# Kernel tuning notes

Hardware: AMD Instinct MI355X
Metric: run time of the kernel (lower is better)

Reference implementation:

```python
import jax, jax.numpy as jnp
import numpy as np

B, T, D, H = 4, 2048, 2048, 16
HD = D // H  # 128
EPS = 1e-5


def setup_inputs() -> dict:
    key = jax.random.key(0)
    ks = jax.random.split(key, 16)
    s_in = 1.0 / np.sqrt(D)
    s_ff = 1.0 / np.sqrt(4 * D)
    return {
        "x": jax.random.normal(ks[0], (B, T, D), jnp.float32),
        # per-head q/k/v projections stacked over heads: [H, D, HD]
        "Wq": jax.random.normal(ks[1], (H, D, HD), jnp.float32) * s_in,
        "bq": jnp.zeros((H, HD), jnp.float32),
        "Wk": jax.random.normal(ks[2], (H, D, HD), jnp.float32) * s_in,
        "bk": jnp.zeros((H, HD), jnp.float32),
        "Wv": jax.random.normal(ks[3], (H, D, HD), jnp.float32) * s_in,
        "bv": jnp.zeros((H, HD), jnp.float32),
        # feed-forward
        "W1": jax.random.normal(ks[4], (D, 4 * D), jnp.float32) * s_in,
        "b1": jnp.zeros((4 * D,), jnp.float32),
        "W2": jax.random.normal(ks[5], (4 * D, D), jnp.float32) * s_ff,
        "b2": jnp.zeros((D,), jnp.float32),
        # layer norms
        "g1": jnp.ones((D,), jnp.float32),
        "be1": jnp.zeros((D,), jnp.float32),
        "g2": jnp.ones((D,), jnp.float32),
        "be2": jnp.zeros((D,), jnp.float32),
    }


def _layernorm(x, g, b):
    mu = jnp.mean(x, axis=-1, keepdims=True)
    var = jnp.mean(jnp.square(x - mu), axis=-1, keepdims=True)
    return (x - mu) * jax.lax.rsqrt(var + EPS) * g + b


def reference(x, Wq, bq, Wk, bk, Wv, bv, W1, b1, W2, b2, g1, be1, g2, be2):
    h = _layernorm(x, g1, be1)
    # per-head projections: [B, H, T, HD]
    q = jnp.einsum("btd,hde->bhte", h, Wq) + bq[None, :, None, :]
    k = jnp.einsum("btd,hde->bhte", h, Wk) + bk[None, :, None, :]
    v = jnp.einsum("btd,hde->bhte", h, Wv) + bv[None, :, None, :]
    scale = 1.0 / jnp.sqrt(jnp.asarray(HD, q.dtype))
    logits = jnp.einsum("bhte,bhse->bhts", q, k) * scale  # [B,H,T,T]
    causal = jnp.tril(jnp.ones((T, T), bool))
    logits = jnp.where(causal[None, None], logits, -jnp.inf)
    attn = jax.nn.softmax(logits, axis=-1)
    out = jnp.einsum("bhts,bhse->bhte", attn, v)  # [B,H,T,HD]
    # concat heads in head order -> [B,T,D]
    out = out.transpose(0, 2, 1, 3).reshape(B, T, D)
    x = x + out
    h2 = _layernorm(x, g2, be2)
    ff = jax.nn.relu(h2 @ W1 + b1) @ W2 + b2
    return x + ff
```

## Files before the change

### kernel.cpp

```cpp
#include <hip/hip_runtime.h>
#include <stdint.h>

#define TLEN 2048
#define DDIM 2048
#define NHEAD 16
#define HDIM 128
#define BSZ 4

typedef short bf16x8 __attribute__((ext_vector_type(8)));
typedef float f32x4 __attribute__((ext_vector_type(4)));

__device__ __forceinline__ unsigned short f32_bf16(float f) {
  union { float f; unsigned int u; } v; v.f = f;
  unsigned int u = v.u;
  unsigned int r = (u + 0x7fffu + ((u >> 16) & 1u)) >> 16;
  return (unsigned short)r;
}

__device__ __forceinline__ void async_cp16(const void* g, void* l) {
  __builtin_amdgcn_global_load_lds(
      (const __attribute__((address_space(1))) unsigned int*)g,
      (__attribute__((address_space(3))) unsigned int*)l, 16, 0, 0);
}

__global__ __launch_bounds__(256) void transpose_bf16_kernel(
    const float* __restrict__ in, unsigned short* __restrict__ out,
    int R, int C, long in_z, long out_z) {
  __shared__ float tile[32][33];
  in += (long)blockIdx.z * in_z;
  out += (long)blockIdx.z * out_z;
  int c0 = blockIdx.x * 32, r0 = blockIdx.y * 32;
  int cr = threadIdx.x & 31, rr = threadIdx.x >> 5;
#pragma unroll
  for (int i = 0; i < 4; ++i)
    tile[rr + i * 8][cr] = in[(long)(r0 + rr + i * 8) * C + c0 + cr];
  __syncthreads();
#pragma unroll
  for (int i = 0; i < 4; ++i)
    out[(long)(c0 + rr + i * 8) * R + r0 + cr] = f32_bf16(tile[cr][rr + i * 8]);
}

__device__ __forceinline__ void block_reduce2(float& s, float& q) {
#pragma unroll
  for (int off = 32; off >= 1; off >>= 1) {
    s += __shfl_xor(s, off);
    q += __shfl_xor(q, off);
  }
  __shared__ float rs[4], rq[4];
  int lane = threadIdx.x & 63, wid = threadIdx.x >> 6;
  if (lane == 0) { rs[wid] = s; rq[wid] = q; }
  __syncthreads();
  s = rs[0] + rs[1] + rs[2] + rs[3];
  q = rq[0] + rq[1] + rq[2] + rq[3];
}

__global__ __launch_bounds__(256) void ln_kernel(
    const float* __restrict__ x, const float* __restrict__ g,
    const float* __restrict__ be, unsigned short* __restrict__ hb) {
  int row = blockIdx.x, tid = threadIdx.x;
  const float* xr = x + (long)row * DDIM;
  float4 v0 = *(const float4*)(xr + tid * 4);
  float4 v1 = *(const float4*)(xr + 1024 + tid * 4);
  float s = v0.x + v0.y + v0.z + v0.w + v1.x + v1.y + v1.z + v1.w;
  float q = v0.x * v0.x + v0.y * v0.y + v0.z * v0.z + v0.w * v0.w +
            v1.x * v1.x + v1.y * v1.y + v1.z * v1.z + v1.w * v1.w;
  block_reduce2(s, q);
  float mu = s * (1.0f / DDIM);
  float var = q * (1.0f / DDIM) - mu * mu;
  float rstd = rsqrtf(var + 1e-5f);
  float4 g0 = *(const float4*)(g + tid * 4);
  float4 g1v = *(const float4*)(g + 1024 + tid * 4);
  float4 b0 = *(const float4*)(be + tid * 4);
  float4 b1v = *(const float4*)(be + 1024 + tid * 4);
  ushort4 o0, o1;
  o0.x = f32_bf16((v0.x - mu) * rstd * g0.x + b0.x);
  o0.y = f32_bf16((v0.y - mu) * rstd * g0.y + b0.y);
  o0.z = f32_bf16((v0.z - mu) * rstd * g0.z + b0.z);
  o0.w = f32_bf16((v0.w - mu) * rstd * g0.w + b0.w);
  o1.x = f32_bf16((v1.x - mu) * rstd * g1v.x + b1v.x);
  o1.y = f32_bf16((v1.y - mu) * rstd * g1v.y + b1v.y);
  o1.z = f32_bf16((v1.z - mu) * rstd * g1v.z + b1v.z);
  o1.w = f32_bf16((v1.w - mu) * rstd * g1v.w + b1v.w);
  *(ushort4*)(hb + (long)row * DDIM + tid * 4) = o0;
  *(ushort4*)(hb + (long)row * DDIM + 1024 + tid * 4) = o1;
}

__global__ __launch_bounds__(256) void resid_ln_kernel(
    const float* __restrict__ x, float* xa,
    const float* __restrict__ g, const float* __restrict__ be,
    unsigned short* __restrict__ hb) {
  int row = blockIdx.x, tid = threadIdx.x;
  const float* xr = x + (long)row * DDIM;
  float* ar = xa + (long)row * DDIM;
  float4 v0 = *(const float4*)(xr + tid * 4);
  float4 a0 = *(const float4*)(ar + tid * 4);
  float4 v1 = *(const float4*)(xr + 1024 + tid * 4);
  float4 a1 = *(const float4*)(ar + 1024 + tid * 4);
  v0.x += a0.x; v0.y += a0.y; v0.z += a0.z; v0.w += a0.w;
  v1.x += a1.x; v1.y += a1.y; v1.z += a1.z; v1.w += a1.w;
  *(float4*)(ar + tid * 4) = v0;
  *(float4*)(ar + 1024 + tid * 4) = v1;
  float s = v0.x + v0.y + v0.z + v0.w + v1.x + v1.y + v1.z + v1.w;
  float q = v0.x * v0.x + v0.y * v0.y + v0.z * v0.z + v0.w * v0.w +
            v1.x * v1.x + v1.y * v1.y + v1.z * v1.z + v1.w * v1.w;
  block_reduce2(s, q);
  float mu = s * (1.0f / DDIM);
  float var = q * (1.0f / DDIM) - mu * mu;
  float rstd = rsqrtf(var + 1e-5f);
  float4 g0 = *(const float4*)(g + tid * 4);
  float4 g1v = *(const float4*)(g + 1024 + tid * 4);
  float4 b0 = *(const float4*)(be + tid * 4);
  float4 b1v = *(const float4*)(be + 1024 + tid * 4);
  ushort4 o0, o1;
  o0.x = f32_bf16((v0.x - mu) * rstd * g0.x + b0.x);
  o0.y = f32_bf16((v0.y - mu) * rstd * g0.y + b0.y);
  o0.z = f32_bf16((v0.z - mu) * rstd * g0.z + b0.z);
  o0.w = f32_bf16((v0.w - mu) * rstd * g0.w + b0.w);
  o1.x = f32_bf16((v1.x - mu) * rstd * g1v.x + b1v.x);
  o1.y = f32_bf16((v1.y - mu) * rstd * g1v.y + b1v.y);
  o1.z = f32_bf16((v1.z - mu) * rstd * g1v.z + b1v.z);
  o1.w = f32_bf16((v1.w - mu) * rstd * g1v.w + b1v.w);
  *(ushort4*)(hb + (long)row * DDIM + tid * 4) = o0;
  *(ushort4*)(hb + (long)row * DDIM + 1024 + tid * 4) = o1;
}

__device__ __forceinline__ void gemm_core(const unsigned short* __restrict__ A,
                                          const unsigned short* __restrict__ Bt,
                                          int K, int lda, int ldb, int m0, int n0,
                                          f32x4 acc[4][4]) {
  __shared__ unsigned short sA[128 * 64];
  __shared__ unsigned short sB[128 * 64];
  const int tid = threadIdx.x;
  const int lane = tid & 63, wid = tid >> 6;
  const int wm = (wid & 1) * 64, wn = (wid >> 1) * 64;
  const int lm = lane & 15, lq = lane >> 4;
#pragma unroll
  for (int mi = 0; mi < 4; ++mi)
#pragma unroll
    for (int ni = 0; ni < 4; ++ni)
      acc[mi][ni] = (f32x4){0.f, 0.f, 0.f, 0.f};
  const int rbase = wid * 32;
  const int ri = lane >> 3;
  const int kgl = lane & 7;
  const int nk = K >> 6;
  for (int kt = 0; kt < nk; ++kt) {
    const unsigned short* Ak = A + (long)m0 * lda + (long)kt * 64;
    const unsigned short* Bk = Bt + (long)n0 * ldb + (long)kt * 64;
#pragma unroll
    for (int ins = 0; ins < 4; ++ins) {
      int row = rbase + ins * 8 + ri;
      int kg = kgl ^ (row & 7);
      async_cp16(Ak + (long)row * lda + kg * 8, &sA[(rbase + ins * 8) * 64]);
      async_cp16(Bk + (long)row * ldb + kg * 8, &sB[(rbase + ins * 8) * 64]);
    }
    __syncthreads();
#pragma unroll
    for (int kc = 0; kc < 2; ++kc) {
      bf16x8 af[4], bfr[4];
#pragma unroll
      for (int mi = 0; mi < 4; ++mi) {
        int row = wm + mi * 16 + lm;
        int kg = (kc * 4 + lq) ^ (row & 7);
        af[mi] = *(const bf16x8*)(&sA[row * 64 + kg * 8]);
      }
#pragma unroll
      for (int ni = 0; ni < 4; ++ni) {
        int row = wn + ni * 16 + lm;
        int kg = (kc * 4 + lq) ^ (row & 7);
        bfr[ni] = *(const bf16x8*)(&sB[row * 64 + kg * 8]);
      }
#pragma unroll
      for (int mi = 0; mi < 4; ++mi)
#pragma unroll
        for (int ni = 0; ni < 4; ++ni)
          acc[mi][ni] = __builtin_amdgcn_mfma_f32_16x16x32_bf16(af[mi], bfr[ni], acc[mi][ni], 0, 0, 0);
    }
    __syncthreads();
  }
}

__global__ __launch_bounds__(256) void gemm_qkv_kernel(
    const unsigned short* __restrict__ A, const unsigned short* __restrict__ WT,
    unsigned short* __restrict__ Qb, unsigned short* __restrict__ Kb,
    unsigned short* __restrict__ VTb,
    const float* __restrict__ bq, const float* __restrict__ bk,
    const float* __restrict__ bv) {
  int m0 = blockIdx.x * 128, n0 = blockIdx.y * 128;
  int z = blockIdx.z;
  const unsigned short* Bt = WT + (long)z * DDIM * DDIM;
  f32x4 acc[4][4];
  gemm_core(A, Bt, DDIM, DDIM, DDIM, m0, n0, acc);
  const float* bias = (z == 0) ? bq : (z == 1) ? bk : bv;
  int lane = threadIdx.x & 63, wid = threadIdx.x >> 6;
  int wm = (wid & 1) * 64, wn = (wid >> 1) * 64, lm = lane & 15, lq = lane >> 4;
  int h = n0 >> 7;
#pragma unroll
  for (int mi = 0; mi < 4; ++mi) {
    int rowb = m0 + wm + mi * 16 + lq * 4;
    int b = rowb >> 11, t0 = rowb & (TLEN - 1);
#pragma unroll
    for (int ni = 0; ni < 4; ++ni) {
      int col = n0 + wn + ni * 16 + lm;
      int e = col & (HDIM - 1);
      float bsv = bias[col];
      if (z < 2) {
        unsigned short* o = (z == 0) ? Qb : Kb;
        long base = ((long)(b * NHEAD + h) * TLEN + t0) * HDIM + e;
#pragma unroll
        for (int r = 0; r < 4; ++r)
          o[base + (long)r * HDIM] = f32_bf16(acc[mi][ni][r] + bsv);
      } else {
        long base = ((long)(b * NHEAD + h) * HDIM + e) * TLEN + t0;
        ushort4 pk;
        pk.x = f32_bf16(acc[mi][ni][0] + bsv);
        pk.y = f32_bf16(acc[mi][ni][1] + bsv);
        pk.z = f32_bf16(acc[mi][ni][2] + bsv);
        pk.w = f32_bf16(acc[mi][ni][3] + bsv);
        *(ushort4*)(VTb + base) = pk;
      }
    }
  }
}

template <int MODE>
__global__ __launch_bounds__(256) void gemm_ffn_kernel(
    const unsigned short* __restrict__ A, const unsigned short* __restrict__ Bt,
    void* __restrict__ outv, const float* __restrict__ bias,
    int K, int lda, int ldb, int N) {
  int m0 = blockIdx.x * 128, n0 = blockIdx.y * 128;
  f32x4 acc[4][4];
  gemm_core(A, Bt, K, lda, ldb, m0, n0, acc);
  int lane = threadIdx.x & 63, wid = threadIdx.x >> 6;
  int wm = (wid & 1) * 64, wn = (wid >> 1) * 64, lm = lane & 15, lq = lane >> 4;
#pragma unroll
  for (int mi = 0; mi < 4; ++mi) {
    int rowb = m0 + wm + mi * 16 + lq * 4;
#pragma unroll
    for (int ni = 0; ni < 4; ++ni) {
      int col = n0 + wn + ni * 16 + lm;
      float bsv = (MODE == 2) ? 0.f : bias[col];
#pragma unroll
      for (int r = 0; r < 4; ++r) {
        long idx = (long)(rowb + r) * N + col;
        float v = acc[mi][ni][r] + bsv;
        if (MODE == 0) {
          ((unsigned short*)outv)[idx] = f32_bf16(v > 0.f ? v : 0.f);
        } else {
          float* o = (float*)outv;
          o[idx] = o[idx] + v;
        }
      }
    }
  }
}

__global__ __launch_bounds__(256, 3) void attn_kernel(
    const unsigned short* __restrict__ Qb, const unsigned short* __restrict__ Kb,
    const unsigned short* __restrict__ VTb, float* __restrict__ Ob) {
  __shared__ __align__(16) char smem[49152];
  unsigned short* kbuf0 = (unsigned short*)smem;
  unsigned short* kbuf1 = (unsigned short*)(smem + 16384);
  unsigned short* sV = (unsigned short*)(smem + 32768);
  const int tid = threadIdx.x, lane = tid & 63, wid = tid >> 6;
  const int lm = lane & 15, lq = lane >> 4;
  int flat = blockIdx.x;
  int swz = (flat & 7) * 256 + (flat >> 3);
  int m5 = swz & 31;
  int bxx = (m5 & 1) ? (m5 >> 1) : (31 - (m5 >> 1));
  int h = (swz >> 5) & 15;
  int b = swz >> 9;
  const int q0 = bxx * 64;
  const long bh = (long)(b * NHEAD + h);
  const unsigned short* qp = Qb + (bh * TLEN + q0 + wid * 16) * HDIM;
  const unsigned short* kp = Kb + bh * TLEN * HDIM;
  const unsigned short* vp = VTb + bh * HDIM * TLEN;
  bf16x8 qf[4];
#pragma unroll
  for (int c = 0; c < 4; ++c)
    qf[c] = *(const bf16x8*)(qp + (long)lm * HDIM + c * 32 + lq * 8);
  f32x4 oacc[8];
#pragma unroll
  for (int c = 0; c < 8; ++c) oacc[c] = (f32x4){0.f, 0.f, 0.f, 0.f};
  float mr[4], lr[4];
#pragma unroll
  for (int r = 0; r < 4; ++r) { mr[r] = -3.0e38f; lr[r] = 0.f; }
  const float sl = 0.08838834764831845f * 1.4426950408889634f;
  const int nk = bxx + 1;
  const int kri = lane >> 4, krg = lane & 15;
  const int vri = lane >> 3, vrg = lane & 7;
#pragma unroll
  for (int i = 0; i < 4; ++i) {
    int row = wid * 16 + i * 4 + kri;
    async_cp16(kp + (long)row * HDIM + (krg ^ (row & 7)) * 8,
               kbuf0 + (wid * 16 + i * 4) * 128);
  }
  for (int it = 0; it < nk; ++it) {
    const int kb = it * 64;
    unsigned short* kc_ = (it & 1) ? kbuf1 : kbuf0;
    unsigned short* kn_ = (it & 1) ? kbuf0 : kbuf1;
    __asm__ volatile("s_waitcnt vmcnt(0)" ::: "memory");
    __asm__ volatile("s_barrier" ::: "memory");
#pragma unroll
    for (int i = 0; i < 4; ++i) {
      int row = wid * 32 + i * 8 + vri;
      async_cp16(vp + (long)row * TLEN + kb + (vrg ^ (row & 7)) * 8,
                 sV + (wid * 32 + i * 8) * 64);
    }
    if (it + 1 < nk) {
      const unsigned short* kp1 = kp + (long)(kb + 64) * HDIM;
#pragma unroll
      for (int i = 0; i < 4; ++i) {
        int row = wid * 16 + i * 4 + kri;
        async_cp16(kp1 + (long)row * HDIM + (krg ^ (row & 7)) * 8,
                   kn_ + (wid * 16 + i * 4) * 128);
      }
    }
    f32x4 s[4];
#pragma unroll
    for (int ni = 0; ni < 4; ++ni) s[ni] = (f32x4){0.f, 0.f, 0.f, 0.f};
    __builtin_amdgcn_s_setprio(1);
#pragma unroll
    for (int c = 0; c < 4; ++c) {
      bf16x8 bk[4];
#pragma unroll
      for (int ni = 0; ni < 4; ++ni) {
        int row = ni * 16 + lm;
        int g = (c * 4 + lq) ^ (row & 7);
        bk[ni] = *(const bf16x8*)(&kc_[row * 128 + g * 8]);
      }
#pragma unroll
      for (int ni = 0; ni < 4; ++ni)
        s[ni] = __builtin_amdgcn_mfma_f32_16x16x32_bf16(qf[c], bk[ni], s[ni], 0, 0, 0);
    }
    __builtin_amdgcn_s_setprio(0);
    const bool diag = (it == nk - 1);
    float v[4][4], pmax[4];
#pragma unroll
    for (int r = 0; r < 4; ++r) {
      int qrow = q0 + wid * 16 + lq * 4 + r;
      float m = -3.0e38f;
#pragma unroll
      for (int ni = 0; ni < 4; ++ni) {
        float t = s[ni][r] * sl;
        if (diag && (kb + ni * 16 + lm > qrow)) t = -3.0e38f;
        v[r][ni] = t;
        m = fmaxf(m, t);
      }
      pmax[r] = m;
    }
    bool need = (pmax[0] > mr[0] + 8.f) | (pmax[1] > mr[1] + 8.f) |
                (pmax[2] > mr[2] + 8.f) | (pmax[3] > mr[3] + 8.f);
    if (__any(need)) {
#pragma unroll
      for (int r = 0; r < 4; ++r) {
        float m = pmax[r];
#pragma unroll
        for (int off = 8; off >= 1; off >>= 1) m = fmaxf(m, __shfl_xor(m, off));
        float mn = fmaxf(mr[r], m);
        float a = exp2f(mr[r] - mn);
        mr[r] = mn;
        lr[r] *= a;
#pragma unroll
        for (int c = 0; c < 8; ++c) oacc[c][r] *= a;
      }
    }
    float p[4][4];
#pragma unroll
    for (int r = 0; r < 4; ++r) {
      float rs = 0.f;
#pragma unroll
      for (int ni = 0; ni < 4; ++ni) {
        p[r][ni] = exp2f(v[r][ni] - mr[r]);
        rs += p[r][ni];
      }
      lr[r] += rs;
    }
    if (it + 1 < nk) {
      __asm__ volatile("s_waitcnt vmcnt(4)" ::: "memory");
    } else {
      __asm__ volatile("s_waitcnt vmcnt(0)" ::: "memory");
    }
    __asm__ volatile("s_barrier" ::: "memory");
    unsigned short* pw = kc_ + wid * 1024;
#pragma unroll
    for (int r = 0; r < 4; ++r) {
      int prow = lq * 4 + r;
#pragma unroll
      for (int ni = 0; ni < 4; ++ni)
        pw[prow * 64 + ((ni * 16 + lm) ^ ((prow & 7) << 3))] = f32_bf16(p[r][ni]);
    }
    __asm__ volatile("s_waitcnt lgkmcnt(0)" ::: "memory");
    __builtin_amdgcn_sched_barrier(0);
    __builtin_amdgcn_s_setprio(1);
#pragma unroll
    for (int kc = 0; kc < 2; ++kc) {
      bf16x8 pf = *(const bf16x8*)(&pw[lm * 64 + ((kc * 32 + lq * 8) ^ ((lm & 7) << 3))]);
#pragma unroll
      for (int c = 0; c < 8; ++c) {
        int row = c * 16 + lm;
        int g = (kc * 4 + lq) ^ (row & 7);
        bf16x8 vf = *(const bf16x8*)(&sV[row * 64 + g * 8]);
        oacc[c] = __builtin_amdgcn_mfma_f32_16x16x32_bf16(pf, vf, oacc[c], 0, 0, 0);
      }
    }
    __builtin_amdgcn_s_setprio(0);
  }
  __syncthreads();
#pragma unroll
  for (int r = 0; r < 4; ++r) {
#pragma unroll
    for (int off = 8; off >= 1; off >>= 1) lr[r] += __shfl_xor(lr[r], off);
  }
  float inv[4];
#pragma unroll
  for (int r = 0; r < 4; ++r) inv[r] = 1.f / lr[r];
  float* sO = (float*)smem;
#pragma unroll
  for (int c = 0; c < 8; ++c)
#pragma unroll
    for (int r = 0; r < 4; ++r)
      sO[(wid * 16 + lq * 4 + r) * 132 + c * 16 + lm] = oacc[c][r] * inv[r];
  __syncthreads();
  float* ob = Ob + ((long)b * TLEN + q0) * DDIM + (long)h * HDIM;
#pragma unroll
  for (int i = 0; i < 8; ++i) {
    int idx = i * 256 + tid;
    int row = idx >> 5, c4 = (idx & 31) * 4;
    *(float4*)(ob + (long)row * DDIM + c4) = *(const float4*)(&sO[row * 132 + c4]);
  }
}

extern "C" void kernel_launch(void* const* d_in, const int* in_sizes, int n_in,
                              void* d_out, int out_size, void* d_ws, size_t ws_size,
                              hipStream_t stream) {
  const float* x   = (const float*)d_in[0];
  const float* Wq  = (const float*)d_in[1];
  const float* bq  = (const float*)d_in[2];
  const float* Wk  = (const float*)d_in[3];
  const float* bk  = (const float*)d_in[4];
  const float* Wv  = (const float*)d_in[5];
  const float* bv  = (const float*)d_in[6];
  const float* W1  = (const float*)d_in[7];
  const float* b1  = (const float*)d_in[8];
  const float* W2  = (const float*)d_in[9];
  const float* b2  = (const float*)d_in[10];
  const float* g1  = (const float*)d_in[11];
  const float* be1 = (const float*)d_in[12];
  const float* g2  = (const float*)d_in[13];
  const float* be2 = (const float*)d_in[14];
  float* out = (float*)d_out;
  char* ws = (char*)d_ws;
  unsigned short* wtqkv  = (unsigned short*)(ws + 0L);
  unsigned short* qb     = (unsigned short*)(ws + 25165824L);
  unsigned short* kbuf   = (unsigned short*)(ws + 58720256L);
  unsigned short* vtb    = (unsigned short*)(ws + 92274688L);
  unsigned short* hbf    = (unsigned short*)(ws + 125829120L);
  unsigned short* ff1buf = qb;
  unsigned short* wt1    = kbuf;
  unsigned short* wt2    = vtb;

  dim3 blk(256);
  transpose_bf16_kernel<<<dim3(4, 64, 16), blk, 0, stream>>>(Wq, wtqkv, 2048, 128, 2048L * 128, 2048L * 128);
  transpose_bf16_kernel<<<dim3(4, 64, 16), blk, 0, stream>>>(Wk, wtqkv + 2048L * 2048, 2048, 128, 2048L * 128, 2048L * 128);
  transpose_bf16_kernel<<<dim3(4, 64, 16), blk, 0, stream>>>(Wv, wtqkv + 2L * 2048 * 2048, 2048, 128, 2048L * 128, 2048L * 128);

  ln_kernel<<<dim3(8192), blk, 0, stream>>>(x, g1, be1, hbf);
  gemm_qkv_kernel<<<dim3(64, 16, 3), blk, 0, stream>>>(hbf, wtqkv, qb, kbuf, vtb, bq, bk, bv);
  attn_kernel<<<dim3(2048), blk, 0, stream>>>(qb, kbuf, vtb, out);

  transpose_bf16_kernel<<<dim3(256, 64, 1), blk, 0, stream>>>(W1, wt1, 2048, 8192, 0, 0);
  transpose_bf16_kernel<<<dim3(64, 256, 1), blk, 0, stream>>>(W2, wt2, 8192, 2048, 0, 0);

  resid_ln_kernel<<<dim3(8192), blk, 0, stream>>>(x, out, g2, be2, hbf);

  for (int s = 0; s < 4; ++s) {
    gemm_ffn_kernel<0><<<dim3(64, 16), blk, 0, stream>>>(
        hbf, wt1 + (long)s * 2048 * 2048, ff1buf, b1 + s * 2048,
        2048, 2048, 2048, 2048);
    if (s == 0) {
      gemm_ffn_kernel<1><<<dim3(64, 16), blk, 0, stream>>>(
          ff1buf, wt2 + (long)s * 2048, out, b2, 2048, 2048, 8192, 2048);
    } else {
      gemm_ffn_kernel<2><<<dim3(64, 16), blk, 0, stream>>>(
          ff1buf, wt2 + (long)s * 2048, out, b2, 2048, 2048, 8192, 2048);
    }
  }
}
```

Baseline: 1.527 ms.

## Double-buffer GEMM LDS tiles to overlap async loads with MFMA compute

The shared GEMM core now keeps two LDS buffers for the A and B tiles. It issues the global-to-LDS loads for the next K tile before computing on the current one, with a single wait-and-barrier per iteration instead of two syncthreads. This is meant to hide global load latency behind the MFMA work. It also raises wave priority around the compute section. In exchange, LDS use doubles, which may reduce occupancy.

```diff
diff --git a/kernel.cpp b/kernel.cpp
--- a/kernel.cpp
+++ b/kernel.cpp
@@ -128,8 +128,8 @@
                                           const unsigned short* __restrict__ Bt,
                                           int K, int lda, int ldb, int m0, int n0,
                                           f32x4 acc[4][4]) {
-  __shared__ unsigned short sA[128 * 64];
-  __shared__ unsigned short sB[128 * 64];
+  __shared__ unsigned short sA[2][128 * 64];
+  __shared__ unsigned short sB[2][128 * 64];
   const int tid = threadIdx.x;
   const int lane = tid & 63, wid = tid >> 6;
   const int wm = (wid & 1) * 64, wn = (wid >> 1) * 64;
@@ -143,17 +143,31 @@
   const int ri = lane >> 3;
   const int kgl = lane & 7;
   const int nk = K >> 6;
+  const unsigned short* Abase = A + (long)m0 * lda;
+  const unsigned short* Bbase = Bt + (long)n0 * ldb;
+#pragma unroll
+  for (int ins = 0; ins < 4; ++ins) {
+    int row = rbase + ins * 8 + ri;
+    int kg = kgl ^ (row & 7);
+    async_cp16(Abase + (long)row * lda + kg * 8, &sA[0][(rbase + ins * 8) * 64]);
+    async_cp16(Bbase + (long)row * ldb + kg * 8, &sB[0][(rbase + ins * 8) * 64]);
+  }
   for (int kt = 0; kt < nk; ++kt) {
-    const unsigned short* Ak = A + (long)m0 * lda + (long)kt * 64;
-    const unsigned short* Bk = Bt + (long)n0 * ldb + (long)kt * 64;
-#pragma unroll
-    for (int ins = 0; ins < 4; ++ins) {
-      int row = rbase + ins * 8 + ri;
-      int kg = kgl ^ (row & 7);
-      async_cp16(Ak + (long)row * lda + kg * 8, &sA[(rbase + ins * 8) * 64]);
-      async_cp16(Bk + (long)row * ldb + kg * 8, &sB[(rbase + ins * 8) * 64]);
-    }
-    __syncthreads();
+    const int cur = kt & 1;
+    __asm__ volatile("s_waitcnt vmcnt(0)" ::: "memory");
+    __asm__ volatile("s_barrier" ::: "memory");
+    if (kt + 1 < nk) {
+      const unsigned short* Ak = Abase + (long)(kt + 1) * 64;
+      const unsigned short* Bk = Bbase + (long)(kt + 1) * 64;
+#pragma unroll
+      for (int ins = 0; ins < 4; ++ins) {
+        int row = rbase + ins * 8 + ri;
+        int kg = kgl ^ (row & 7);
+        async_cp16(Ak + (long)row * lda + kg * 8, &sA[cur ^ 1][(rbase + ins * 8) * 64]);
+        async_cp16(Bk + (long)row * ldb + kg * 8, &sB[cur ^ 1][(rbase + ins * 8) * 64]);
+      }
+    }
+    __builtin_amdgcn_s_setprio(1);
 #pragma unroll
     for (int kc = 0; kc < 2; ++kc) {
       bf16x8 af[4], bfr[4];
@@ -161,13 +175,13 @@
       for (int mi = 0; mi < 4; ++mi) {
         int row = wm + mi * 16 + lm;
         int kg = (kc * 4 + lq) ^ (row & 7);
-        af[mi] = *(const bf16x8*)(&sA[row * 64 + kg * 8]);
+        af[mi] = *(const bf16x8*)(&sA[cur][row * 64 + kg * 8]);
       }
 #pragma unroll
       for (int ni = 0; ni < 4; ++ni) {
         int row = wn + ni * 16 + lm;
         int kg = (kc * 4 + lq) ^ (row & 7);
-        bfr[ni] = *(const bf16x8*)(&sB[row * 64 + kg * 8]);
+        bfr[ni] = *(const bf16x8*)(&sB[cur][row * 64 + kg * 8]);
       }
 #pragma unroll
       for (int mi = 0; mi < 4; ++mi)
@@ -175,7 +189,7 @@
         for (int ni = 0; ni < 4; ++ni)
           acc[mi][ni] = __builtin_amdgcn_mfma_f32_16x16x32_bf16(af[mi], bfr[ni], acc[mi][ni], 0, 0, 0);
     }
-    __syncthreads();
+    __builtin_amdgcn_s_setprio(0);
   }
 }
 
```

After: 1.463 ms. -4.2%, faster.
